# Kernel optimization log

Hardware: AMD Instinct MI355X
Metric: run time of the kernel (lower is better)

The kernel has to match this reference:

```python
import jax, jax.numpy as jnp
import numpy as np

T = 2048        # tokens
HID = 4096      # hidden_size
H = 32          # num attention heads
KV = 8          # num key/value heads (GQA)
D = HID // H    # head_dim = 128
THETA = 10000.0


def setup_inputs() -> dict:
    key = jax.random.key(0)
    k1, k2, k3 = jax.random.split(key, 3)
    hidden_states = jax.random.normal(k1, (T, HID), jnp.float32)
    positions = jnp.arange(T, dtype=jnp.int32)
    Wqkv = jax.random.normal(k2, ((H + 2 * KV) * D, HID), jnp.float32) * 0.02
    Wo = jax.random.normal(k3, (HID, H * D), jnp.float32) * 0.02
    return {"hidden_states": hidden_states, "positions": positions,
            "Wqkv": Wqkv, "Wo": Wo}


def _rope(positions, x):
    """Neox-style rotary embedding. x: [T, h, D], positions: [T]."""
    half = D // 2
    inv_freq = 1.0 / (THETA ** (jnp.arange(half, dtype=jnp.float32) / half))
    ang = positions.astype(jnp.float32)[:, None] * inv_freq      # [T, half]
    cos = jnp.cos(ang)[:, None, :]                                # [T, 1, half]
    sin = jnp.sin(ang)[:, None, :]
    x1, x2 = x[..., :half], x[..., half:]
    return jnp.concatenate([x1 * cos - x2 * sin, x2 * cos + x1 * sin], axis=-1)


def reference(hidden_states, positions, Wqkv, Wo):
    # fused QKV projection (no bias)
    qkv = hidden_states @ Wqkv.T                                  # [T, (H+2KV)*D]
    q, k, v = jnp.split(qkv, [H * D, H * D + KV * D], axis=1)
    q = q.reshape(T, H, D)
    k = k.reshape(T, KV, D)
    v = v.reshape(T, KV, D)
    # RoPE on q and k
    q = _rope(positions, q)
    k = _rope(positions, k)
    # GQA: expand kv heads to match q heads
    g = H // KV
    k = jnp.repeat(k, g, axis=1)                                  # [T, H, D]
    v = jnp.repeat(v, g, axis=1)
    # causal attention (flash-attention math)
    scores = jnp.einsum('thd,shd->hts', q, k) * (D ** -0.5)       # [H, T, T]
    causal = jnp.tril(jnp.ones((T, T), dtype=bool))
    scores = jnp.where(causal[None], scores, jnp.float32(-1e30))
    probs = jax.nn.softmax(scores, axis=-1)
    attn = jnp.einsum('hts,shd->thd', probs, v).reshape(T, H * D)
    # output projection
    return attn @ Wo.T
```

## Files before the change

kernel.cpp:

```cpp
#include <hip/hip_runtime.h>
#include <stdint.h>

#define T_SEQ 2048
#define HIDDEN 4096
#define NHEAD 32
#define NKV 8
#define HDIM 128
#define QKVN 6144

typedef __bf16 bf16x8 __attribute__((ext_vector_type(8)));
typedef float f32x4 __attribute__((ext_vector_type(4)));
typedef unsigned short u16;
typedef u16 u16x8 __attribute__((ext_vector_type(8)));
typedef u16 u16x4 __attribute__((ext_vector_type(4)));

__device__ __forceinline__ u16 f2bf(float f) {
  uint32_t u = __builtin_bit_cast(uint32_t, f);
  u = (u + 0x7fffu + ((u >> 16) & 1u)) >> 16;
  return (u16)u;
}
__device__ __forceinline__ float bf2f(u16 h) {
  uint32_t u = ((uint32_t)h) << 16;
  return __builtin_bit_cast(float, u);
}

__device__ __forceinline__ void gload16(const void* g, void* l) {
  __builtin_amdgcn_global_load_lds(
      (__attribute__((address_space(1))) void*)(uintptr_t)g,
      (__attribute__((address_space(3))) void*)(uintptr_t)l, 16, 0, 0);
}

__global__ void cvt2_kernel(const float* __restrict__ in1, u16* __restrict__ out1, int n1_4,
                            const float* __restrict__ in2, u16* __restrict__ out2, int n2_4) {
  int base = blockIdx.x * blockDim.x + threadIdx.x;
  int stride = gridDim.x * blockDim.x;
  for (int i = base; i < n1_4; i += stride) {
    float4 v = ((const float4*)in1)[i];
    u16x4 o;
    o.x = f2bf(v.x); o.y = f2bf(v.y); o.z = f2bf(v.z); o.w = f2bf(v.w);
    ((u16x4*)out1)[i] = o;
  }
  for (int i = base; i < n2_4; i += stride) {
    float4 v = ((const float4*)in2)[i];
    u16x4 o;
    o.x = f2bf(v.x); o.y = f2bf(v.y); o.z = f2bf(v.z); o.w = f2bf(v.w);
    ((u16x4*)out2)[i] = o;
  }
}

__global__ void prep_kernel(u16* __restrict__ qkv, const int* __restrict__ pos,
                            u16* __restrict__ vt,
                            const float* __restrict__ wo_in, u16* __restrict__ wo_out,
                            int wo_n4) {
  __shared__ u16 tile[64][64];
  const int bid = blockIdx.x;
  const int tid = threadIdx.x;

  if (bid < 512) {
    const int tb = bid & 31;
    const int yy = bid >> 5;
    const int kvh = yy >> 1;
    const int d0 = (yy & 1) * 64;
    const u16* src = qkv + (size_t)(NHEAD + NKV) * HDIM + kvh * HDIM + d0;
#pragma unroll
    for (int g = 0; g < 2; ++g) {
      int u = g * 256 + tid;
      int t = u >> 3, ds = u & 7;
      u16x8 v = *(const u16x8*)(src + (size_t)(tb * 64 + t) * QKVN + ds * 8);
#pragma unroll
      for (int j = 0; j < 8; ++j) {
        int d = ds * 8 + j;
        tile[d][(((t >> 3) ^ (d & 7)) * 8) + (t & 7)] = v[j];
      }
    }
    __syncthreads();
    u16* dst = vt + ((size_t)kvh * HDIM + d0) * T_SEQ + tb * 64;
#pragma unroll
    for (int g = 0; g < 4; ++g) {
      int u = g * 256 + tid;
      int d = u >> 4, qd = u & 15;
      int a = qd >> 3, gg = (qd >> 1) & 3, b = qd & 1;
      int t0 = 32 * a + 16 * b + 4 * gg;
      u16x4 v = *(const u16x4*)&tile[d][(((t0 >> 3) ^ (d & 7)) * 8) + (t0 & 7)];
      *(u16x4*)(dst + (size_t)d * T_SEQ + qd * 4) = v;
    }
    return;
  }

  const int nb = gridDim.x - 512;
  const int base = (bid - 512) * blockDim.x + tid;
  const int stride = nb * blockDim.x;
  for (int idx = base; idx < T_SEQ * 40 * 64; idx += stride) {
    int i = idx & 63;
    int head = (idx >> 6) % 40;
    int t = idx / (40 * 64);
    int hb = head < NHEAD ? head * HDIM : NHEAD * HDIM + (head - NHEAD) * HDIM;
    float p = (float)pos[t];
    float inv_freq = exp2f(-(float)i * (13.287712379549449f / 64.0f));
    float ang = p * inv_freq;
    float s, c;
    sincosf(ang, &s, &c);
    u16* p1 = qkv + (size_t)t * QKVN + hb + i;
    u16* p2 = p1 + 64;
    float x1 = bf2f(*p1), x2 = bf2f(*p2);
    *p1 = f2bf(x1 * c - x2 * s);
    *p2 = f2bf(x2 * c + x1 * s);
  }
  for (int i = base; i < wo_n4; i += stride) {
    float4 v = ((const float4*)wo_in)[i];
    u16x4 o;
    o.x = f2bf(v.x); o.y = f2bf(v.y); o.z = f2bf(v.z); o.w = f2bf(v.w);
    ((u16x4*)wo_out)[i] = o;
  }
}

__device__ __forceinline__ void storeC(float* p, float v) { *p = v; }
__device__ __forceinline__ void storeC(u16* p, float v) { *p = f2bf(v); }
__device__ __forceinline__ f32x4 mfma16(bf16x8 a, bf16x8 b, f32x4 c) {
  return __builtin_amdgcn_mfma_f32_16x16x32_bf16(a, b, c, 0, 0, 0);
}

__global__ void __launch_bounds__(512, 1)
gemm_qkv(const u16* __restrict__ A, const u16* __restrict__ B,
         u16* __restrict__ C, int M, int N, int K) {
  __shared__ u16 As_[2][128 * 64];
  __shared__ u16 Bs_[2][384 * 64];

  const int tid = threadIdx.x;
  const int lane = tid & 63;
  const int w = tid >> 6;
  const int wr = w >> 2, wc = w & 3;
  const int l15 = lane & 15, lg = lane >> 4;

  const int c8 = blockIdx.x & 7, i8 = blockIdx.x >> 3;
  const int by = i8 & 15;
  const int bx = c8 * 2 + (i8 >> 4);
  const int bm = by * 128, bn = bx * 384;

  const int u_lo = w * 64 + lane, u_hi = u_lo + 512;
  const int r0 = u_lo >> 3, s0 = (u_lo & 7) ^ (r0 & 7);
  const int r1 = u_hi >> 3, s1 = (u_hi & 7) ^ (r1 & 7);
  const u16* a_s0 = A + (size_t)(bm + r0) * K + s0 * 8;
  const u16* a_s1 = A + (size_t)(bm + r1) * K + s1 * 8;
  const u16* b_s0[3];
  const u16* b_s1[3];
#pragma unroll
  for (int h = 0; h < 3; ++h) {
    b_s0[h] = B + (size_t)(bn + h * 128 + r0) * K + s0 * 8;
    b_s1[h] = B + (size_t)(bn + h * 128 + r1) * K + s1 * 8;
  }

  const int ax = l15 & 7;
  const int sl0 = (lg ^ ax) * 8;
  const int sl1 = ((4 + lg) ^ ax) * 8;
  const int a_row = (wr * 64 + l15) * 64;
  const int b_row = (wc * 96 + l15) * 64;

  f32x4 acc[4][6] = {};
  bf16x8 bfr[6][2];

#define BARRIER() asm volatile("s_barrier" ::: "memory")
#define WAITBAR(n_) asm volatile("s_waitcnt vmcnt(" #n_ ")\n\ts_barrier" ::: "memory")
#define STAGE_A(t_, p_)                                                        \
  {                                                                            \
    gload16(a_s0 + (size_t)(t_) * 64, &As_[p_][w * 512]);                      \
    gload16(a_s1 + (size_t)(t_) * 64, &As_[p_][4096 + w * 512]);               \
  }
#define STAGE_B(t_, p_, h_)                                                    \
  {                                                                            \
    gload16(b_s0[h_] + (size_t)(t_) * 64, &Bs_[p_][(h_) * 8192 + w * 512]);    \
    gload16(b_s1[h_] + (size_t)(t_) * 64,                                      \
            &Bs_[p_][(h_) * 8192 + 4096 + w * 512]);                           \
  }

  STAGE_A(0, 0);
  STAGE_B(0, 0, 0); STAGE_B(0, 0, 1); STAGE_B(0, 0, 2);
  STAGE_B(1, 1, 0); STAGE_B(1, 1, 1); STAGE_B(1, 1, 2);
  WAITBAR(6);

  const int NT = K >> 6;
  for (int v = 0; v < NT; ++v) {
    const int cur = v & 1, alt = cur ^ 1;
    const u16* Ac = &As_[cur][0];
    const u16* Bc = &Bs_[cur][0];
    const bool s1ok = (v + 1) < NT, s2ok = (v + 2) < NT;

#define MFMA_PH(mi_, A0_, A1_)                                                 \
    __builtin_amdgcn_s_setprio(1);                                             \
    _Pragma("unroll") for (int ni = 0; ni < 6; ++ni) {                         \
      acc[mi_][ni] = mfma16(A0_, bfr[ni][0], acc[mi_][ni]);                    \
      acc[mi_][ni] = mfma16(A1_, bfr[ni][1], acc[mi_][ni]);                    \
    }                                                                          \
    __builtin_amdgcn_s_setprio(0);

    {
      if (s1ok) STAGE_A(v + 1, alt);
#pragma unroll
      for (int ni = 0; ni < 6; ++ni) {
        bfr[ni][0] = *(const bf16x8*)&Bc[b_row + ni * 1024 + sl0];
        bfr[ni][1] = *(const bf16x8*)&Bc[b_row + ni * 1024 + sl1];
      }
      bf16x8 a0 = *(const bf16x8*)&Ac[a_row + 0 * 1024 + sl0];
      bf16x8 a1 = *(const bf16x8*)&Ac[a_row + 0 * 1024 + sl1];
      BARRIER();
      MFMA_PH(0, a0, a1);
      BARRIER();
    }
    {
      if (s2ok) STAGE_B(v + 2, cur, 0);
      bf16x8 a0 = *(const bf16x8*)&Ac[a_row + 1 * 1024 + sl0];
      bf16x8 a1 = *(const bf16x8*)&Ac[a_row + 1 * 1024 + sl1];
      BARRIER();
      MFMA_PH(1, a0, a1);
      BARRIER();
    }
    {
      if (s2ok) STAGE_B(v + 2, cur, 1);
      bf16x8 a0 = *(const bf16x8*)&Ac[a_row + 2 * 1024 + sl0];
      bf16x8 a1 = *(const bf16x8*)&Ac[a_row + 2 * 1024 + sl1];
      BARRIER();
      MFMA_PH(2, a0, a1);
      BARRIER();
    }
    {
      if (s2ok) STAGE_B(v + 2, cur, 2);
      bf16x8 a0 = *(const bf16x8*)&Ac[a_row + 3 * 1024 + sl0];
      bf16x8 a1 = *(const bf16x8*)&Ac[a_row + 3 * 1024 + sl1];
      BARRIER();
      MFMA_PH(3, a0, a1);
      if (s2ok) { WAITBAR(6); } else if (s1ok) { WAITBAR(0); } else { BARRIER(); }
    }
#undef MFMA_PH
  }

#pragma unroll
  for (int mi = 0; mi < 4; ++mi)
#pragma unroll
    for (int ni = 0; ni < 6; ++ni)
#pragma unroll
      for (int r = 0; r < 4; ++r) {
        int row = bm + wr * 64 + mi * 16 + lg * 4 + r;
        int col = bn + wc * 96 + ni * 16 + l15;
        storeC(&C[(size_t)row * N + col], acc[mi][ni][r]);
      }
#undef STAGE_A
#undef STAGE_B
#undef WAITBAR
#undef BARRIER
}

template <typename OutT>
__global__ void __launch_bounds__(512, 2)
gemm256(const u16* __restrict__ A, const u16* __restrict__ B,
        OutT* __restrict__ C0, OutT* __restrict__ C1,
        int N, int K, int NT, int sliceBlocks,
        int nbx, int rw, int rh) {
  __shared__ u16 As_[2][256 * 64];
  __shared__ u16 Bs_[2][256 * 64];

  const int tid = threadIdx.x;
  const int lane = tid & 63;
  const int w = tid >> 6;
  const int wr = w >> 2, wc = w & 3;
  const int l15 = lane & 15, lg = lane >> 4;

  const int bid = blockIdx.x;
  const int slice = bid / sliceBlocks;
  const int wi = bid % sliceBlocks;
  const int k0 = slice * (NT << 6);
  OutT* __restrict__ C = slice ? C1 : C0;

  const int c8 = wi & 7, i8 = wi >> 3;
  const int rpr = nbx / rw;
  const int by = (c8 / rpr) * rh + (i8 % rh);
  const int bx = (c8 % rpr) * rw + (i8 / rh);
  const int bm = by * 256, bn = bx * 256;

  const int u_lo = w * 64 + lane, u_hi = u_lo + 512;
  const int r0 = u_lo >> 3, s0 = (u_lo & 7) ^ (r0 & 7);
  const int r1 = u_hi >> 3, s1 = (u_hi & 7) ^ (r1 & 7);
  const u16* a0s0 = A + (size_t)(bm + r0) * K + k0 + s0 * 8;
  const u16* a0s1 = A + (size_t)(bm + r1) * K + k0 + s1 * 8;
  const u16* a1s0 = A + (size_t)(bm + 128 + r0) * K + k0 + s0 * 8;
  const u16* a1s1 = A + (size_t)(bm + 128 + r1) * K + k0 + s1 * 8;
  const u16* b0s0 = B + (size_t)(bn + r0) * K + k0 + s0 * 8;
  const u16* b0s1 = B + (size_t)(bn + r1) * K + k0 + s1 * 8;
  const u16* b1s0 = B + (size_t)(bn + 128 + r0) * K + k0 + s0 * 8;
  const u16* b1s1 = B + (size_t)(bn + 128 + r1) * K + k0 + s1 * 8;

  const int ax = l15 & 7;
  const int sl0 = (lg ^ ax) * 8;
  const int sl1 = ((4 + lg) ^ ax) * 8;
  const int a_row = (wr * 128 + l15) * 64;
  const int b_row = (wc * 64 + l15) * 64;

  f32x4 acc[8][4] = {};
  bf16x8 bfr[4][2];

#define BARRIER() asm volatile("s_barrier" ::: "memory")
#define WAITBAR(n_) asm volatile("s_waitcnt vmcnt(" #n_ ")\n\ts_barrier" ::: "memory")
#define STAGE_HALF(p0_, p1_, dst_, t_)                                         \
  {                                                                            \
    gload16((p0_) + (size_t)(t_) * 64, (dst_) + (size_t)w * 512);              \
    gload16((p1_) + (size_t)(t_) * 64, (dst_) + 4096 + (size_t)w * 512);       \
  }

  STAGE_HALF(a0s0, a0s1, &As_[0][0], 0);
  STAGE_HALF(a1s0, a1s1, &As_[0][8192], 0);
  STAGE_HALF(b0s0, b0s1, &Bs_[0][0], 0);
  STAGE_HALF(b1s0, b1s1, &Bs_[0][8192], 0);
  STAGE_HALF(b0s0, b0s1, &Bs_[1][0], 1);
  STAGE_HALF(b1s0, b1s1, &Bs_[1][8192], 1);
  WAITBAR(4);

  for (int v = 0; v < NT; ++v) {
    const int cur = v & 1, alt = cur ^ 1;
    const u16* Ac = &As_[cur][0];
    const u16* Bc = &Bs_[cur][0];
    const bool s1ok = (v + 1) < NT, s2ok = (v + 2) < NT;

#define MFMA_QUAD(p_, A0_, A1_, A2_, A3_)                                      \
    __builtin_amdgcn_s_setprio(1);                                             \
    _Pragma("unroll") for (int ni = 0; ni < 4; ++ni) {                         \
      acc[2 * (p_)][ni] = mfma16(A0_, bfr[ni][0], acc[2 * (p_)][ni]);          \
      acc[2 * (p_)][ni] = mfma16(A1_, bfr[ni][1], acc[2 * (p_)][ni]);          \
      acc[2 * (p_) + 1][ni] = mfma16(A2_, bfr[ni][0], acc[2 * (p_) + 1][ni]);  \
      acc[2 * (p_) + 1][ni] = mfma16(A3_, bfr[ni][1], acc[2 * (p_) + 1][ni]);  \
    }                                                                          \
    __builtin_amdgcn_s_setprio(0);

    {
#pragma unroll
      for (int ni = 0; ni < 4; ++ni) {
        bfr[ni][0] = *(const bf16x8*)&Bc[b_row + ni * 1024 + sl0];
        bfr[ni][1] = *(const bf16x8*)&Bc[b_row + ni * 1024 + sl1];
      }
      bf16x8 f0 = *(const bf16x8*)&Ac[a_row + 0 * 1024 + sl0];
      bf16x8 f1 = *(const bf16x8*)&Ac[a_row + 0 * 1024 + sl1];
      bf16x8 f2 = *(const bf16x8*)&Ac[a_row + 1 * 1024 + sl0];
      bf16x8 f3 = *(const bf16x8*)&Ac[a_row + 1 * 1024 + sl1];
      if (s1ok) STAGE_HALF(a0s0, a0s1, &As_[alt][0], v + 1);
      BARRIER();
      MFMA_QUAD(0, f0, f1, f2, f3);
      BARRIER();
    }
    {
      bf16x8 f0 = *(const bf16x8*)&Ac[a_row + 2 * 1024 + sl0];
      bf16x8 f1 = *(const bf16x8*)&Ac[a_row + 2 * 1024 + sl1];
      bf16x8 f2 = *(const bf16x8*)&Ac[a_row + 3 * 1024 + sl0];
      bf16x8 f3 = *(const bf16x8*)&Ac[a_row + 3 * 1024 + sl1];
      if (s1ok) STAGE_HALF(a1s0, a1s1, &As_[alt][8192], v + 1);
      if (s2ok) STAGE_HALF(b0s0, b0s1, &Bs_[cur][0], v + 2);
      BARRIER();
      MFMA_QUAD(1, f0, f1, f2, f3);
      BARRIER();
    }
    {
      bf16x8 f0 = *(const bf16x8*)&Ac[a_row + 4 * 1024 + sl0];
      bf16x8 f1 = *(const bf16x8*)&Ac[a_row + 4 * 1024 + sl1];
      bf16x8 f2 = *(const bf16x8*)&Ac[a_row + 5 * 1024 + sl0];
      bf16x8 f3 = *(const bf16x8*)&Ac[a_row + 5 * 1024 + sl1];
      if (s2ok) STAGE_HALF(b1s0, b1s1, &Bs_[cur][8192], v + 2);
      BARRIER();
      MFMA_QUAD(2, f0, f1, f2, f3);
      BARRIER();
    }
    {
      bf16x8 f0 = *(const bf16x8*)&Ac[a_row + 6 * 1024 + sl0];
      bf16x8 f1 = *(const bf16x8*)&Ac[a_row + 6 * 1024 + sl1];
      bf16x8 f2 = *(const bf16x8*)&Ac[a_row + 7 * 1024 + sl0];
      bf16x8 f3 = *(const bf16x8*)&Ac[a_row + 7 * 1024 + sl1];
      BARRIER();
      MFMA_QUAD(3, f0, f1, f2, f3);
      if (s2ok) { WAITBAR(4); } else { WAITBAR(0); }
    }
#undef MFMA_QUAD
  }

#pragma unroll
  for (int mi = 0; mi < 8; ++mi)
#pragma unroll
    for (int ni = 0; ni < 4; ++ni)
#pragma unroll
      for (int r = 0; r < 4; ++r) {
        int row = bm + wr * 128 + mi * 16 + lg * 4 + r;
        int col = bn + wc * 64 + ni * 16 + l15;
        storeC(&C[(size_t)row * N + col], acc[mi][ni][r]);
      }
#undef STAGE_HALF
#undef WAITBAR
#undef BARRIER
}

__global__ void reduce_add(float* __restrict__ out, const float* __restrict__ part, int n4) {
  int i = blockIdx.x * blockDim.x + threadIdx.x;
  int stride = gridDim.x * blockDim.x;
  for (; i < n4; i += stride) {
    float4 a = ((const float4*)out)[i];
    float4 b = ((const float4*)part)[i];
    a.x += b.x; a.y += b.y; a.z += b.z; a.w += b.w;
    ((float4*)out)[i] = a;
  }
}

__global__ void __launch_bounds__(256, 2)
attn_kernel(const u16* __restrict__ qkv, const u16* __restrict__ vt,
            u16* __restrict__ out) {
  __shared__ u16 Ksh[2][64 * 128];
  __shared__ u16 Vsh[2][128 * 64];

  const int tid = threadIdx.x;
  const int lane = tid & 63;
  const int w = tid >> 6;
  const int l15 = lane & 15, lg = lane >> 4;

  const int bid = blockIdx.x;
  const int u8 = bid & 255, sfl = bid >> 8;
  const int kvh = u8 & 7;
  const int hg = (u8 >> 3) & 3;
  const int x = (u8 >> 5) & 7;
  const int qi = sfl ? x : (15 - x);
  const int h = kvh * 4 + hg;
  const int q0 = qi * 128;
  const int nt = 2 * qi + 2;
  const int wrow = q0 + w * 32;

  const u16* Kg = qkv + NHEAD * HDIM + kvh * HDIM;
  const u16* Vg = vt + (size_t)kvh * HDIM * T_SEQ;

  bf16x8 qa[2][4];
#pragma unroll
  for (int mi = 0; mi < 2; ++mi) {
    const u16* qrow = qkv + (size_t)(wrow + mi * 16 + l15) * QKVN + h * HDIM + lg * 8;
#pragma unroll
    for (int ks = 0; ks < 4; ++ks) qa[mi][ks] = *(const bf16x8*)(qrow + ks * 32);
  }

  f32x4 acc_o[2][8] = {};
  float m[2] = {-1e30f, -1e30f}, lsum[2] = {0.f, 0.f};

  const float scale = 0.088388347648318447f;

#define STAGE_K(kv0, p)                                                        \
  {                                                                            \
    _Pragma("unroll") for (int rnd = 0; rnd < 4; ++rnd) {                      \
      int cc = rnd * 256 + tid;                                                \
      int krow = cc >> 4, kslot = cc & 15;                                     \
      gload16(Kg + (size_t)((kv0) + krow) * QKVN + (kslot ^ (krow & 7)) * 8,   \
              &Ksh[p][(rnd * 256 + w * 64) * 8]);                              \
    }                                                                          \
  }
#define STAGE_V(kv0, p)                                                        \
  {                                                                            \
    _Pragma("unroll") for (int rnd = 0; rnd < 4; ++rnd) {                      \
      int cc = rnd * 256 + tid;                                                \
      int vrow = cc >> 3, ps = cc & 7;                                         \
      gload16(Vg + (size_t)vrow * T_SEQ + (kv0) + ((ps ^ (vrow & 7)) * 8),     \
              &Vsh[p][(rnd * 256 + w * 64) * 8]);                              \
    }                                                                          \
  }

  STAGE_K(0, 0);
  STAGE_V(0, 0);
  __syncthreads();

  for (int t = 0; t < nt; ++t) {
    const int p = t & 1;
    const int kv0 = t * 64;
    const bool more = (t + 1 < nt);
    if (more) {
      STAGE_K(kv0 + 64, p ^ 1);
      STAGE_V(kv0 + 64, p ^ 1);
    }

    if (kv0 <= wrow + 31) {
      f32x4 s[2][4] = {};
#pragma unroll
      for (int ks = 0; ks < 4; ++ks) {
#pragma unroll
        for (int n = 0; n < 4; ++n) {
          int row16 = n * 16 + l15;
          bf16x8 kf = *(const bf16x8*)&Ksh[p][row16 * 128 +
                                              (((ks * 4 + lg) ^ (row16 & 7)) * 8)];
          s[0][n] = mfma16(kf, qa[0][ks], s[0][n]);
          s[1][n] = mfma16(kf, qa[1][ks], s[1][n]);
        }
      }

      const bool diag = (kv0 + 63 > wrow);
      float mx[2];
#pragma unroll
      for (int mi = 0; mi < 2; ++mi) {
        float mm = -1e30f;
        int tq = wrow + mi * 16 + l15;
#pragma unroll
        for (int n = 0; n < 4; ++n)
#pragma unroll
          for (int r = 0; r < 4; ++r) {
            float v = s[mi][n][r] * scale;
            if (diag && (kv0 + n * 16 + lg * 4 + r) > tq) v = -1e30f;
            s[mi][n][r] = v;
            mm = fmaxf(mm, v);
          }
        mm = fmaxf(mm, __shfl_xor(mm, 16, 64));
        mm = fmaxf(mm, __shfl_xor(mm, 32, 64));
        mx[mi] = mm;
      }

      float alpha[2];
#pragma unroll
      for (int mi = 0; mi < 2; ++mi) {
        float mn = fmaxf(m[mi], mx[mi]);
        alpha[mi] = __expf(m[mi] - mn);
        m[mi] = mn;
        lsum[mi] *= alpha[mi];
      }
#pragma unroll
      for (int mi = 0; mi < 2; ++mi)
#pragma unroll
        for (int r = 0; r < 4; ++r) {
          float al = __shfl(alpha[mi], lg * 4 + r, 64);
#pragma unroll
          for (int nd = 0; nd < 8; ++nd) acc_o[mi][nd][r] *= al;
        }

      bf16x8 paf[2][2];
#pragma unroll
      for (int mi = 0; mi < 2; ++mi) {
        float ps = 0.f;
#pragma unroll
        for (int n = 0; n < 4; ++n)
#pragma unroll
          for (int r = 0; r < 4; ++r) {
            float pv = __expf(s[mi][n][r] - m[mi]);
            s[mi][n][r] = pv;
            ps += pv;
          }
        ps += __shfl_xor(ps, 16, 64);
        ps += __shfl_xor(ps, 32, 64);
        lsum[mi] += ps;
#pragma unroll
        for (int ks = 0; ks < 2; ++ks) {
          u16x8 pk;
#pragma unroll
          for (int hn = 0; hn < 2; ++hn)
#pragma unroll
            for (int r = 0; r < 4; ++r)
              pk[hn * 4 + r] = f2bf(s[mi][2 * ks + hn][r]);
          paf[mi][ks] = __builtin_bit_cast(bf16x8, pk);
        }
      }

#pragma unroll
      for (int ks = 0; ks < 2; ++ks) {
#pragma unroll
        for (int nd = 0; nd < 8; ++nd) {
          int d = nd * 16 + l15;
          bf16x8 bv = *(const bf16x8*)&Vsh[p][d * 64 + (((ks * 4 + lg) ^ (d & 7)) * 8)];
          acc_o[0][nd] = mfma16(paf[0][ks], bv, acc_o[0][nd]);
          acc_o[1][nd] = mfma16(paf[1][ks], bv, acc_o[1][nd]);
        }
      }
    }

    __syncthreads();
  }

#pragma unroll
  for (int mi = 0; mi < 2; ++mi)
#pragma unroll
    for (int r = 0; r < 4; ++r) {
      float ls = __shfl(lsum[mi], lg * 4 + r, 64);
      float inv = 1.f / ls;
      int row = wrow + mi * 16 + lg * 4 + r;
#pragma unroll
      for (int nd = 0; nd < 8; ++nd) {
        int col = h * HDIM + nd * 16 + l15;
        out[(size_t)row * (NHEAD * HDIM) + col] = f2bf(acc_o[mi][nd][r] * inv);
      }
    }
#undef STAGE_K
#undef STAGE_V
}

extern "C" void kernel_launch(void* const* d_in, const int* in_sizes, int n_in,
                              void* d_out, int out_size, void* d_ws, size_t ws_size,
                              hipStream_t stream) {
  const float* hs   = (const float*)d_in[0];
  const int*   pos  = (const int*)d_in[1];
  const float* wqkv = (const float*)d_in[2];
  const float* wo   = (const float*)d_in[3];
  float* out = (float*)d_out;
  uint8_t* ws = (uint8_t*)d_ws;

  if (ws_size < 142606336u) return;
  u16* hs_bf   = (u16*)(ws + 0);
  u16* wqkv_bf = (u16*)(ws + 16777216u);
  u16* wo_bf   = (u16*)(ws + 67108864u);
  u16* qkv_bf  = (u16*)(ws + 100663296u);
  u16* attn_bf = (u16*)(ws + 125829120u);
  float* part  = (float*)(ws + 16777216u);
  u16* vt_buf  = (u16*)(ws + 0);

  cvt2_kernel<<<2048, 256, 0, stream>>>(hs, hs_bf, (T_SEQ * HIDDEN) / 4,
                                        wqkv, wqkv_bf, (QKVN * HIDDEN) / 4);

  gemm_qkv<<<256, 512, 0, stream>>>(hs_bf, wqkv_bf, qkv_bf, T_SEQ, QKVN, HIDDEN);

  prep_kernel<<<2048, 256, 0, stream>>>(qkv_bf, pos, vt_buf,
                                        wo, wo_bf, (HIDDEN * HIDDEN) / 4);

  attn_kernel<<<512, 256, 0, stream>>>(qkv_bf, vt_buf, attn_bf);

  gemm256<float><<<256, 512, 0, stream>>>(
      attn_bf, wo_bf, out, part, HIDDEN, HIDDEN, 32, 128, 16, 2, 8);

  reduce_add<<<2048, 256, 0, stream>>>(out, part, (T_SEQ * HIDDEN) / 4);
}
```

Baseline: 317.7 us.

## Restructure QKV GEMM inner loop from four MFMA phases into three

The per-K-tile schedule of the large GEMM kernel is reorganized from four phases of one A row-block by six B column-blocks into three phases: 2x3, 2x3, then 2x6 MFMA blocks. All three B-tile global prefetches are now issued together in the last phase instead of one per phase. The aim is fewer barriers per iteration and more MFMAs between LDS reads. In exchange it keeps more A fragments live in registers and bunches the global loads into one burst, which may hurt latency hiding or occupancy.

```diff
diff --git a/kernel.cpp b/kernel.cpp
--- a/kernel.cpp
+++ b/kernel.cpp
@@ -157,7 +157,7 @@
   const int b_row = (wc * 96 + l15) * 64;
 
   f32x4 acc[4][6] = {};
-  bf16x8 bfr[6][2];
+  bf16x8 af[4][2], bfr[6][2];
 
 #define BARRIER() asm volatile("s_barrier" ::: "memory")
 #define WAITBAR(n_) asm volatile("s_waitcnt vmcnt(" #n_ ")\n\ts_barrier" ::: "memory")
@@ -185,52 +185,67 @@
     const u16* Bc = &Bs_[cur][0];
     const bool s1ok = (v + 1) < NT, s2ok = (v + 2) < NT;
 
-#define MFMA_PH(mi_, A0_, A1_)                                                 \
-    __builtin_amdgcn_s_setprio(1);                                             \
-    _Pragma("unroll") for (int ni = 0; ni < 6; ++ni) {                         \
-      acc[mi_][ni] = mfma16(A0_, bfr[ni][0], acc[mi_][ni]);                    \
-      acc[mi_][ni] = mfma16(A1_, bfr[ni][1], acc[mi_][ni]);                    \
-    }                                                                          \
-    __builtin_amdgcn_s_setprio(0);
-
     {
       if (s1ok) STAGE_A(v + 1, alt);
 #pragma unroll
-      for (int ni = 0; ni < 6; ++ni) {
+      for (int mi = 0; mi < 2; ++mi) {
+        af[mi][0] = *(const bf16x8*)&Ac[a_row + mi * 1024 + sl0];
+        af[mi][1] = *(const bf16x8*)&Ac[a_row + mi * 1024 + sl1];
+      }
+#pragma unroll
+      for (int ni = 0; ni < 3; ++ni) {
         bfr[ni][0] = *(const bf16x8*)&Bc[b_row + ni * 1024 + sl0];
         bfr[ni][1] = *(const bf16x8*)&Bc[b_row + ni * 1024 + sl1];
       }
-      bf16x8 a0 = *(const bf16x8*)&Ac[a_row + 0 * 1024 + sl0];
-      bf16x8 a1 = *(const bf16x8*)&Ac[a_row + 0 * 1024 + sl1];
-      BARRIER();
-      MFMA_PH(0, a0, a1);
+      BARRIER();
+      __builtin_amdgcn_s_setprio(1);
+#pragma unroll
+      for (int mi = 0; mi < 2; ++mi)
+#pragma unroll
+        for (int ni = 0; ni < 3; ++ni) {
+          acc[mi][ni] = mfma16(af[mi][0], bfr[ni][0], acc[mi][ni]);
+          acc[mi][ni] = mfma16(af[mi][1], bfr[ni][1], acc[mi][ni]);
+        }
+      __builtin_amdgcn_s_setprio(0);
       BARRIER();
     }
     {
-      if (s2ok) STAGE_B(v + 2, cur, 0);
-      bf16x8 a0 = *(const bf16x8*)&Ac[a_row + 1 * 1024 + sl0];
-      bf16x8 a1 = *(const bf16x8*)&Ac[a_row + 1 * 1024 + sl1];
-      BARRIER();
-      MFMA_PH(1, a0, a1);
+#pragma unroll
+      for (int ni = 3; ni < 6; ++ni) {
+        bfr[ni][0] = *(const bf16x8*)&Bc[b_row + ni * 1024 + sl0];
+        bfr[ni][1] = *(const bf16x8*)&Bc[b_row + ni * 1024 + sl1];
+      }
+      BARRIER();
+      __builtin_amdgcn_s_setprio(1);
+#pragma unroll
+      for (int mi = 0; mi < 2; ++mi)
+#pragma unroll
+        for (int ni = 3; ni < 6; ++ni) {
+          acc[mi][ni] = mfma16(af[mi][0], bfr[ni][0], acc[mi][ni]);
+          acc[mi][ni] = mfma16(af[mi][1], bfr[ni][1], acc[mi][ni]);
+        }
+      __builtin_amdgcn_s_setprio(0);
       BARRIER();
     }
     {
-      if (s2ok) STAGE_B(v + 2, cur, 1);
-      bf16x8 a0 = *(const bf16x8*)&Ac[a_row + 2 * 1024 + sl0];
-      bf16x8 a1 = *(const bf16x8*)&Ac[a_row + 2 * 1024 + sl1];
-      BARRIER();
-      MFMA_PH(2, a0, a1);
-      BARRIER();
-    }
-    {
-      if (s2ok) STAGE_B(v + 2, cur, 2);
-      bf16x8 a0 = *(const bf16x8*)&Ac[a_row + 3 * 1024 + sl0];
-      bf16x8 a1 = *(const bf16x8*)&Ac[a_row + 3 * 1024 + sl1];
-      BARRIER();
-      MFMA_PH(3, a0, a1);
+      if (s2ok) { STAGE_B(v + 2, cur, 0); STAGE_B(v + 2, cur, 1); STAGE_B(v + 2, cur, 2); }
+#pragma unroll
+      for (int mi = 2; mi < 4; ++mi) {
+        af[mi][0] = *(const bf16x8*)&Ac[a_row + mi * 1024 + sl0];
+        af[mi][1] = *(const bf16x8*)&Ac[a_row + mi * 1024 + sl1];
+      }
+      BARRIER();
+      __builtin_amdgcn_s_setprio(1);
+#pragma unroll
+      for (int mi = 2; mi < 4; ++mi)
+#pragma unroll
+        for (int ni = 0; ni < 6; ++ni) {
+          acc[mi][ni] = mfma16(af[mi][0], bfr[ni][0], acc[mi][ni]);
+          acc[mi][ni] = mfma16(af[mi][1], bfr[ni][1], acc[mi][ni]);
+        }
+      __builtin_amdgcn_s_setprio(0);
       if (s2ok) { WAITBAR(6); } else if (s1ok) { WAITBAR(0); } else { BARRIER(); }
     }
-#undef MFMA_PH
   }
 
 #pragma unroll
```

New measurement: 318.4 us. Within noise of the previous version (+0.2%).
